# Performance work log

Measured on AMD Instinct MI355X. Metric: run time of the kernel, lower is better.

## Reference

```python
import jax, jax.numpy as jnp
import numpy as np

EPS = 1e-6
QMAX = 127.0  # 8-bit absmax activation quantization (BitNet b1.58 style)


def _quant_weight(W):
    # ternary {-1,0,1} with per-tensor mean-abs scale
    scale = jnp.mean(jnp.abs(W))
    scale = jnp.maximum(scale, EPS)
    q = jnp.clip(jnp.round(W / scale), -1.0, 1.0)
    return q * scale  # dequantized ternary weight


def _quant_act(x):
    # per-token absmax 8-bit quantization over the feature dim
    s = QMAX / jnp.maximum(jnp.max(jnp.abs(x), axis=-1, keepdims=True), EPS)
    q = jnp.clip(jnp.round(x * s), -QMAX - 1.0, QMAX)
    return q / s  # dequantized activation


def setup_inputs() -> dict:
    key = jax.random.key(0)
    k1, k2 = jax.random.split(key)
    B, S, D_IN, D_OUT = 4, 2048, 4096, 4096
    x = jax.random.normal(k1, (B, S, D_IN), dtype=jnp.float32)
    # xavier-uniform-ish weight init
    limit = float(np.sqrt(6.0 / (D_IN + D_OUT)))
    W = jax.random.uniform(k2, (D_OUT, D_IN), dtype=jnp.float32, minval=-limit, maxval=limit)
    b = jnp.zeros((D_OUT,), dtype=jnp.float32)
    return {"x": x, "W": W, "b": b}


def reference(x, W, b):
    dqx = _quant_act(x)      # [B,S,Din]
    dqw = _quant_weight(W)   # [Dout,Din]
    # F.linear: x @ W.T + b
    out = jnp.einsum('bsd,od->bso', dqx, dqw) + b
    return out
```

## Files before the change

kernel.cpp:

```cpp
#include <hip/hip_runtime.h>
#include <hip/hip_bf16.h>
#include <stdint.h>
#include <stddef.h>

#define DIN  4096
#define MTOK 8192
#define NOUT 4096
#define KT   64

typedef __attribute__((ext_vector_type(4))) int   i32x4;
typedef __attribute__((ext_vector_type(4))) float f32x4;

#define OFF_SUM 0
#define OFF_F   256
#define OFF_QX  65536
#define OFF_QW  (65536 + (size_t)MTOK*DIN)


__global__ __launch_bounds__(256) void k_sumabs(const float* __restrict__ W,
                                                double* __restrict__ sum) {
  int idx = blockIdx.x * 256 + threadIdx.x;
  const f32x4* W4 = (const f32x4*)W;
  double s = 0.0;
#pragma unroll
  for (int i = 0; i < 8; ++i) {
    f32x4 v = W4[idx + i * 524288];
    s += (double)fabsf(v[0]) + (double)fabsf(v[1]) +
         (double)fabsf(v[2]) + (double)fabsf(v[3]);
  }
#pragma unroll
  for (int off = 32; off > 0; off >>= 1) s += __shfl_xor(s, off);
  __shared__ double wsum[4];
  int lane = threadIdx.x & 63, w = threadIdx.x >> 6;
  if (lane == 0) wsum[w] = s;
  __syncthreads();
  if (threadIdx.x == 0) atomicAdd(sum, wsum[0] + wsum[1] + wsum[2] + wsum[3]);
}

__global__ __launch_bounds__(256) void k_quant(const float* __restrict__ x,
                                               const float* __restrict__ W,
                                               const double* __restrict__ sum,
                                               char* __restrict__ qX,
                                               char* __restrict__ qW,
                                               float* __restrict__ f) {
  __shared__ float sval[16];
  __shared__ float red[16][4];
  const int blk = blockIdx.x;
  const int t = threadIdx.x;
  const bool isW = (blk < 256);
  const float* src;
  char* dst;
  if (isW) {
    src = W + (size_t)blk * 16 * DIN;
    dst = qW + (size_t)blk * 65536;
  } else {
    src = x + (size_t)(blk - 256) * 16 * DIN;
    dst = qX + (size_t)(blk - 256) * 65536;
  }
  float lo, hi;
  if (isW) {
    if (t < 16) {
      float s = (float)(*sum * (1.0 / 16777216.0));
      if (s < 1e-6f) s = 1e-6f;
      sval[t] = s;
    }
    lo = -1.f; hi = 1.f;
  } else {
    const f32x4* sv = (const f32x4*)src;
    float rmax[16];
#pragma unroll
    for (int r = 0; r < 16; ++r) rmax[r] = 0.f;
#pragma unroll
    for (int i = 0; i < 64; ++i) {
      f32x4 v = sv[i * 256 + t];
      float mm = fmaxf(fmaxf(fabsf(v[0]), fabsf(v[1])),
                       fmaxf(fabsf(v[2]), fabsf(v[3])));
      rmax[i >> 2] = fmaxf(rmax[i >> 2], mm);
    }
    const int lane = t & 63, w = t >> 6;
#pragma unroll
    for (int r = 0; r < 16; ++r) {
      float v = rmax[r];
#pragma unroll
      for (int off = 32; off > 0; off >>= 1) v = fmaxf(v, __shfl_xor(v, off));
      if (lane == 0) red[r][w] = v;
    }
    __syncthreads();
    if (t < 16) {
      float m = fmaxf(fmaxf(red[t][0], red[t][1]), fmaxf(red[t][2], red[t][3]));
      m = fmaxf(m, 1e-6f);
      sval[t] = 127.0f / m;
      f[(blk - 256) * 16 + t] = m * (1.0f / 127.0f);
    }
    lo = -128.f; hi = 127.f;
  }
  __syncthreads();
#pragma unroll 4
  for (int i = 0; i < 64; ++i) {
    const int o = i * 1024 + t * 4;
    const int row = (t >> 2) & 15;
    const int k = i * 64 + (t >> 6) * 16 + (t & 3) * 4;
    f32x4 v = *(const f32x4*)(src + (size_t)row * DIN + k);
    float s = sval[row];
    int q0, q1, q2, q3;
    if (isW) {
      q0 = (int)fminf(fmaxf(rintf(v[0] / s), lo), hi);
      q1 = (int)fminf(fmaxf(rintf(v[1] / s), lo), hi);
      q2 = (int)fminf(fmaxf(rintf(v[2] / s), lo), hi);
      q3 = (int)fminf(fmaxf(rintf(v[3] / s), lo), hi);
    } else {
      q0 = (int)fminf(fmaxf(rintf(v[0] * s), lo), hi);
      q1 = (int)fminf(fmaxf(rintf(v[1] * s), lo), hi);
      q2 = (int)fminf(fmaxf(rintf(v[2] * s), lo), hi);
      q3 = (int)fminf(fmaxf(rintf(v[3] * s), lo), hi);
    }
    uint32_t pk = (uint32_t)(q0 & 255) | ((uint32_t)(q1 & 255) << 8) |
                  ((uint32_t)(q2 & 255) << 16) | ((uint32_t)(q3 & 255) << 24);
    *(uint32_t*)(dst + o) = pk;
  }
}

__device__ __forceinline__ void gload16(const void* g, void* l) {
  __builtin_amdgcn_global_load_lds(
      (const __attribute__((address_space(1))) void*)g,
      (__attribute__((address_space(3))) void*)l, 16, 0, 0);
}

__global__ __launch_bounds__(512, 2) void k_gemm(const char* __restrict__ qX,
                                                 const char* __restrict__ qW,
                                                 const float* __restrict__ f,
                                                 const double* __restrict__ sum,
                                                 const float* __restrict__ bias,
                                                 float* __restrict__ out) {
  const int bid = blockIdx.x;
  const int xcd = bid & 7, slot = bid >> 3;
  const int pass = slot >> 5, q = slot & 31;
  const int mm = q >> 3, nn = q & 7;
  const int pm = xcd >> 1, pn = xcd & 1;
  const int bmi = pass * 16 + pm * 4 + mm;
  const int bni = pn * 8 + nn;
  const int mt0 = bmi * 16;
  const int nt0 = bni * 16;

  __shared__ __align__(16) char lds[4][2][16384];

  const int t = threadIdx.x;
  const int lane = t & 63;
  const int w = t >> 6;
  const int wm = w >> 2, wn = w & 3;

  const char* gA0 = qX + ((size_t)(mt0 + w) * 64) * 1024 + lane * 16;
  const char* gA1 = qX + ((size_t)(mt0 + w + 8) * 64) * 1024 + lane * 16;
  const char* gB0 = qW + ((size_t)(nt0 + w) * 64) * 1024 + lane * 16;
  const char* gB1 = qW + ((size_t)(nt0 + w + 8) * 64) * 1024 + lane * 16;

#define STAGE(buf, kt) do {                                     \
    gload16(gA0 + (size_t)(kt) * 1024, &lds[buf][0][w * 1024]);        \
    gload16(gA1 + (size_t)(kt) * 1024, &lds[buf][0][(w + 8) * 1024]);  \
    gload16(gB0 + (size_t)(kt) * 1024, &lds[buf][1][w * 1024]);        \
    gload16(gB1 + (size_t)(kt) * 1024, &lds[buf][1][(w + 8) * 1024]);  \
  } while (0)

  i32x4 acc[8][4] = {};

  auto compute = [&](int buf) {
    const char* bA = &lds[buf][0][wm * 8192 + lane * 16];
    const char* bB = &lds[buf][1][wn * 4096 + lane * 16];
    i32x4 a[8], b[4];
#pragma unroll
    for (int i = 0; i < 8; ++i) a[i] = *(const i32x4*)(bA + i * 1024);
#pragma unroll
    for (int j = 0; j < 4; ++j) b[j] = *(const i32x4*)(bB + j * 1024);
    __builtin_amdgcn_s_setprio(1);
#pragma unroll
    for (int i = 0; i < 8; ++i)
#pragma unroll
      for (int j = 0; j < 4; ++j)
        acc[i][j] = __builtin_amdgcn_mfma_i32_16x16x64_i8(a[i], b[j], acc[i][j], 0, 0, 0);
    __builtin_amdgcn_s_setprio(0);
  };

  STAGE(0, 0);
  STAGE(1, 1);
  for (int kt = 0; kt < KT - 2; ++kt) {
    STAGE((kt + 2) & 3, kt + 2);
    asm volatile("s_waitcnt vmcnt(8)" ::: "memory");
    __builtin_amdgcn_s_barrier();
    asm volatile("" ::: "memory");
    compute(kt & 3);
  }
  asm volatile("s_waitcnt vmcnt(4)" ::: "memory");
  __builtin_amdgcn_s_barrier();
  asm volatile("" ::: "memory");
  compute((KT - 2) & 3);
  asm volatile("s_waitcnt vmcnt(0)" ::: "memory");
  __builtin_amdgcn_s_barrier();
  asm volatile("" ::: "memory");
  compute((KT - 1) & 3);

  float wsc = (float)(*sum * (1.0 / 16777216.0));
  if (wsc < 1e-6f) wsc = 1e-6f;
  const int col0 = bni * 256 + wn * 64 + (lane & 15);
  const int row0 = bmi * 256 + wm * 128 + ((lane >> 4) << 2);
  float bj[4];
#pragma unroll
  for (int j = 0; j < 4; ++j) bj[j] = bias[col0 + j * 16];
#pragma unroll
  for (int i = 0; i < 8; ++i) {
#pragma unroll
    for (int qr = 0; qr < 4; ++qr) {
      const int m = row0 + i * 16 + qr;
      const float fm = f[m] * wsc;
      float* orow = out + (size_t)m * NOUT;
#pragma unroll
      for (int j = 0; j < 4; ++j)
        orow[col0 + j * 16] = (float)acc[i][j][qr] * fm + bj[j];
    }
  }
#undef STAGE
}

extern "C" void kernel_launch(void* const* d_in, const int* in_sizes, int n_in,
                              void* d_out, int out_size, void* d_ws, size_t ws_size,
                              hipStream_t stream) {
  const float* x    = (const float*)d_in[0];
  const float* W    = (const float*)d_in[1];
  const float* bias = (const float*)d_in[2];
  float* out = (float*)d_out;
  char* ws = (char*)d_ws;

  double* sum = (double*)(ws + OFF_SUM);
  float* f    = (float*)(ws + OFF_F);
  char* qX    = ws + OFF_QX;
  char* qW    = ws + OFF_QW;

  hipMemsetAsync(d_ws, 0, 256, stream);
  k_sumabs<<<2048, 256, 0, stream>>>(W, sum);
  k_quant<<<768, 256, 0, stream>>>(x, W, sum, qX, qW, f);
  k_gemm<<<512, 512, 0, stream>>>(qX, qW, f, sum, bias, out);
}
```

Before: 450.1 us.

## Rewrite quant kernel one-row-per-wave and reschedule GEMM LDS/MFMA pipeline

The quantization kernel now assigns one row per wavefront. Each wave holds its 64 floats per lane in registers, reduces the absmax with shuffles alone instead of through shared memory, and writes 16-byte packed stores into the tiled layout. The GEMM main loop is restructured to load LDS fragments into registers first, then issue the next global-to-LDS stage, wait on lgkmcnt, and run the MFMAs behind a sched_barrier, with a second barrier per iteration. The aim is to overlap fragment reads with prefetch and to cut quant-kernel sync overhead, at the cost of an extra barrier per k-step and higher register pressure.

```diff
diff --git a/kernel.cpp b/kernel.cpp
--- a/kernel.cpp
+++ b/kernel.cpp
@@ -37,86 +37,65 @@
   if (threadIdx.x == 0) atomicAdd(sum, wsum[0] + wsum[1] + wsum[2] + wsum[3]);
 }
 
-__global__ __launch_bounds__(256) void k_quant(const float* __restrict__ x,
-                                               const float* __restrict__ W,
-                                               const double* __restrict__ sum,
-                                               char* __restrict__ qX,
-                                               char* __restrict__ qW,
-                                               float* __restrict__ f) {
-  __shared__ float sval[16];
-  __shared__ float red[16][4];
+__global__ __launch_bounds__(512) void k_quantall(const float* __restrict__ x,
+                                                  const float* __restrict__ W,
+                                                  const double* __restrict__ sum,
+                                                  char* __restrict__ qX,
+                                                  char* __restrict__ qW,
+                                                  float* __restrict__ f) {
+  const int t = threadIdx.x;
+  const int w = t >> 6, lane = t & 63;
   const int blk = blockIdx.x;
-  const int t = threadIdx.x;
-  const bool isW = (blk < 256);
-  const float* src;
-  char* dst;
+  const bool isW = (blk < 512);
+  const int row = isW ? (blk * 8 + w) : ((blk - 512) * 8 + w);
+  const float* src = (isW ? W : x) + (size_t)row * DIN + lane * 64;
+
+  f32x4 v[16];
+#pragma unroll
+  for (int i = 0; i < 16; ++i) v[i] = ((const f32x4*)src)[i];
+
+  float s;
   if (isW) {
-    src = W + (size_t)blk * 16 * DIN;
-    dst = qW + (size_t)blk * 65536;
+    float ws = (float)(*sum * (1.0 / 16777216.0));
+    if (ws < 1e-6f) ws = 1e-6f;
+    s = ws;
   } else {
-    src = x + (size_t)(blk - 256) * 16 * DIN;
-    dst = qX + (size_t)(blk - 256) * 65536;
-  }
-  float lo, hi;
-  if (isW) {
-    if (t < 16) {
-      float s = (float)(*sum * (1.0 / 16777216.0));
-      if (s < 1e-6f) s = 1e-6f;
-      sval[t] = s;
+    float m = 0.f;
+#pragma unroll
+    for (int i = 0; i < 16; ++i)
+      m = fmaxf(m, fmaxf(fmaxf(fabsf(v[i][0]), fabsf(v[i][1])),
+                         fmaxf(fabsf(v[i][2]), fabsf(v[i][3]))));
+#pragma unroll
+    for (int off = 32; off > 0; off >>= 1) m = fmaxf(m, __shfl_xor(m, off));
+    m = fmaxf(m, 1e-6f);
+    if (lane == 0) f[row] = m * (1.0f / 127.0f);
+    s = 127.0f / m;
+  }
+
+  char* dst = (isW ? qW : qX) + (size_t)(row >> 4) * 65536 +
+              (size_t)lane * 1024 + (row & 15) * 16;
+#pragma unroll
+  for (int c = 0; c < 4; ++c) {
+    i32x4 pk;
+#pragma unroll
+    for (int wd = 0; wd < 4; ++wd) {
+      f32x4 u = v[c * 4 + wd];
+      int q0, q1, q2, q3;
+      if (isW) {
+        q0 = (int)fminf(fmaxf(rintf(u[0] / s), -1.f), 1.f);
+        q1 = (int)fminf(fmaxf(rintf(u[1] / s), -1.f), 1.f);
+        q2 = (int)fminf(fmaxf(rintf(u[2] / s), -1.f), 1.f);
+        q3 = (int)fminf(fmaxf(rintf(u[3] / s), -1.f), 1.f);
+      } else {
+        q0 = (int)fminf(fmaxf(rintf(u[0] * s), -128.f), 127.f);
+        q1 = (int)fminf(fmaxf(rintf(u[1] * s), -128.f), 127.f);
+        q2 = (int)fminf(fmaxf(rintf(u[2] * s), -128.f), 127.f);
+        q3 = (int)fminf(fmaxf(rintf(u[3] * s), -128.f), 127.f);
+      }
+      pk[wd] = (int)((uint32_t)(q0 & 255) | ((uint32_t)(q1 & 255) << 8) |
+                     ((uint32_t)(q2 & 255) << 16) | ((uint32_t)(q3 & 255) << 24));
     }
-    lo = -1.f; hi = 1.f;
-  } else {
-    const f32x4* sv = (const f32x4*)src;
-    float rmax[16];
-#pragma unroll
-    for (int r = 0; r < 16; ++r) rmax[r] = 0.f;
-#pragma unroll
-    for (int i = 0; i < 64; ++i) {
-      f32x4 v = sv[i * 256 + t];
-      float mm = fmaxf(fmaxf(fabsf(v[0]), fabsf(v[1])),
-                       fmaxf(fabsf(v[2]), fabsf(v[3])));
-      rmax[i >> 2] = fmaxf(rmax[i >> 2], mm);
-    }
-    const int lane = t & 63, w = t >> 6;
-#pragma unroll
-    for (int r = 0; r < 16; ++r) {
-      float v = rmax[r];
-#pragma unroll
-      for (int off = 32; off > 0; off >>= 1) v = fmaxf(v, __shfl_xor(v, off));
-      if (lane == 0) red[r][w] = v;
-    }
-    __syncthreads();
-    if (t < 16) {
-      float m = fmaxf(fmaxf(red[t][0], red[t][1]), fmaxf(red[t][2], red[t][3]));
-      m = fmaxf(m, 1e-6f);
-      sval[t] = 127.0f / m;
-      f[(blk - 256) * 16 + t] = m * (1.0f / 127.0f);
-    }
-    lo = -128.f; hi = 127.f;
-  }
-  __syncthreads();
-#pragma unroll 4
-  for (int i = 0; i < 64; ++i) {
-    const int o = i * 1024 + t * 4;
-    const int row = (t >> 2) & 15;
-    const int k = i * 64 + (t >> 6) * 16 + (t & 3) * 4;
-    f32x4 v = *(const f32x4*)(src + (size_t)row * DIN + k);
-    float s = sval[row];
-    int q0, q1, q2, q3;
-    if (isW) {
-      q0 = (int)fminf(fmaxf(rintf(v[0] / s), lo), hi);
-      q1 = (int)fminf(fmaxf(rintf(v[1] / s), lo), hi);
-      q2 = (int)fminf(fmaxf(rintf(v[2] / s), lo), hi);
-      q3 = (int)fminf(fmaxf(rintf(v[3] / s), lo), hi);
-    } else {
-      q0 = (int)fminf(fmaxf(rintf(v[0] * s), lo), hi);
-      q1 = (int)fminf(fmaxf(rintf(v[1] * s), lo), hi);
-      q2 = (int)fminf(fmaxf(rintf(v[2] * s), lo), hi);
-      q3 = (int)fminf(fmaxf(rintf(v[3] * s), lo), hi);
-    }
-    uint32_t pk = (uint32_t)(q0 & 255) | ((uint32_t)(q1 & 255) << 8) |
-                  ((uint32_t)(q2 & 255) << 16) | ((uint32_t)(q3 & 255) << 24);
-    *(uint32_t*)(dst + o) = pk;
+    *(i32x4*)(dst + c * 256) = pk;
   }
 }
 
@@ -154,49 +133,61 @@
   const char* gB0 = qW + ((size_t)(nt0 + w) * 64) * 1024 + lane * 16;
   const char* gB1 = qW + ((size_t)(nt0 + w + 8) * 64) * 1024 + lane * 16;
 
-#define STAGE(buf, kt) do {                                     \
+#define STAGE(buf, kt) do {                                            \
     gload16(gA0 + (size_t)(kt) * 1024, &lds[buf][0][w * 1024]);        \
     gload16(gA1 + (size_t)(kt) * 1024, &lds[buf][0][(w + 8) * 1024]);  \
     gload16(gB0 + (size_t)(kt) * 1024, &lds[buf][1][w * 1024]);        \
     gload16(gB1 + (size_t)(kt) * 1024, &lds[buf][1][(w + 8) * 1024]);  \
   } while (0)
 
+#define LOADFRAGS(buf) do {                                            \
+    const char* bA = &lds[buf][0][wm * 8192 + lane * 16];              \
+    const char* bB = &lds[buf][1][wn * 4096 + lane * 16];              \
+    _Pragma("unroll")                                                  \
+    for (int i = 0; i < 8; ++i) a[i] = *(const i32x4*)(bA + i * 1024); \
+    _Pragma("unroll")                                                  \
+    for (int j = 0; j < 4; ++j) b[j] = *(const i32x4*)(bB + j * 1024); \
+  } while (0)
+
+#define MFMAS do {                                                     \
+    __builtin_amdgcn_s_setprio(1);                                     \
+    _Pragma("unroll")                                                  \
+    for (int i = 0; i < 8; ++i)                                        \
+      _Pragma("unroll")                                                \
+      for (int j = 0; j < 4; ++j)                                      \
+        acc[i][j] = __builtin_amdgcn_mfma_i32_16x16x64_i8(a[i], b[j], acc[i][j], 0, 0, 0); \
+    __builtin_amdgcn_s_setprio(0);                                     \
+  } while (0)
+
   i32x4 acc[8][4] = {};
-
-  auto compute = [&](int buf) {
-    const char* bA = &lds[buf][0][wm * 8192 + lane * 16];
-    const char* bB = &lds[buf][1][wn * 4096 + lane * 16];
-    i32x4 a[8], b[4];
-#pragma unroll
-    for (int i = 0; i < 8; ++i) a[i] = *(const i32x4*)(bA + i * 1024);
-#pragma unroll
-    for (int j = 0; j < 4; ++j) b[j] = *(const i32x4*)(bB + j * 1024);
-    __builtin_amdgcn_s_setprio(1);
-#pragma unroll
-    for (int i = 0; i < 8; ++i)
-#pragma unroll
-      for (int j = 0; j < 4; ++j)
-        acc[i][j] = __builtin_amdgcn_mfma_i32_16x16x64_i8(a[i], b[j], acc[i][j], 0, 0, 0);
-    __builtin_amdgcn_s_setprio(0);
-  };
+  i32x4 a[8], b[4];
 
   STAGE(0, 0);
   STAGE(1, 1);
-  for (int kt = 0; kt < KT - 2; ++kt) {
-    STAGE((kt + 2) & 3, kt + 2);
-    asm volatile("s_waitcnt vmcnt(8)" ::: "memory");
-    __builtin_amdgcn_s_barrier();
-    asm volatile("" ::: "memory");
-    compute(kt & 3);
-  }
   asm volatile("s_waitcnt vmcnt(4)" ::: "memory");
   __builtin_amdgcn_s_barrier();
-  asm volatile("" ::: "memory");
-  compute((KT - 2) & 3);
+
+  for (int kt = 0; kt < KT - 2; ++kt) {
+    LOADFRAGS(kt & 3);
+    STAGE((kt + 2) & 3, kt + 2);
+    __builtin_amdgcn_s_barrier();
+    asm volatile("s_waitcnt lgkmcnt(0)" ::: "memory");
+    __builtin_amdgcn_sched_barrier(0);
+    MFMAS;
+    asm volatile("s_waitcnt vmcnt(4)" ::: "memory");
+    __builtin_amdgcn_s_barrier();
+  }
+  LOADFRAGS((KT - 2) & 3);
+  __builtin_amdgcn_s_barrier();
+  asm volatile("s_waitcnt lgkmcnt(0)" ::: "memory");
+  __builtin_amdgcn_sched_barrier(0);
+  MFMAS;
   asm volatile("s_waitcnt vmcnt(0)" ::: "memory");
   __builtin_amdgcn_s_barrier();
-  asm volatile("" ::: "memory");
-  compute((KT - 1) & 3);
+  LOADFRAGS((KT - 1) & 3);
+  asm volatile("s_waitcnt lgkmcnt(0)" ::: "memory");
+  __builtin_amdgcn_sched_barrier(0);
+  MFMAS;
 
   float wsc = (float)(*sum * (1.0 / 16777216.0));
   if (wsc < 1e-6f) wsc = 1e-6f;
@@ -218,6 +209,8 @@
     }
   }
 #undef STAGE
+#undef LOADFRAGS
+#undef MFMAS
 }
 
 extern "C" void kernel_launch(void* const* d_in, const int* in_sizes, int n_in,
@@ -236,6 +229,6 @@
 
   hipMemsetAsync(d_ws, 0, 256, stream);
   k_sumabs<<<2048, 256, 0, stream>>>(W, sum);
-  k_quant<<<768, 256, 0, stream>>>(x, W, sum, qX, qW, f);
+  k_quantall<<<1536, 512, 0, stream>>>(x, W, sum, qX, qW, f);
   k_gemm<<<512, 512, 0, stream>>>(qX, qW, f, sum, bias, out);
 }
```

New measurement: 417.9 us. 7.1% less time.
